# Performance work log

Measured on AMD Instinct MI355X. Metric: run time of the kernel, lower is better.

Reference implementation:

```python
import jax, jax.numpy as jnp
import numpy as np

NUM_LAYERS = 4
HID = 512
BATCH = 32
SEQ = 2048


def log_g(x):
    # log of the g() activation used by minGRU: g(x) = x+0.5 for x>=0, sigmoid(x) for x<0
    return jnp.where(x >= 0, jnp.log(jax.nn.relu(x) + 0.5), -jax.nn.softplus(-x))


def parallel_scan_log(log_coeffs, log_values):
    # log_coeffs: (B, T, H), log_values: (B, T+1, H); returns h: (B, T, H)
    a_star = jnp.cumsum(jnp.pad(log_coeffs, ((0, 0), (1, 0), (0, 0))), axis=1)  # (B, T+1, H)
    log_h = a_star + jax.lax.cumlogsumexp(log_values - a_star, axis=1)
    return jnp.exp(log_h)[:, 1:]


def setup_inputs() -> dict:
    key = jax.random.key(0)
    ks = jax.random.split(key, 4)
    x = jax.random.normal(ks[0], (BATCH, SEQ, HID), dtype=jnp.float32)
    h0 = jax.random.uniform(ks[1], (NUM_LAYERS, BATCH, HID), dtype=jnp.float32)
    scale = 0.02
    Wz = jax.random.normal(ks[2], (NUM_LAYERS, HID, HID), dtype=jnp.float32) * scale
    Wh = jax.random.normal(ks[3], (NUM_LAYERS, HID, HID), dtype=jnp.float32) * scale
    bz = jnp.zeros((NUM_LAYERS, HID), dtype=jnp.float32)
    bh = jnp.zeros((NUM_LAYERS, HID), dtype=jnp.float32)
    gamma = jnp.ones((NUM_LAYERS, HID), dtype=jnp.float32)
    beta = jnp.zeros((NUM_LAYERS, HID), dtype=jnp.float32)
    return {"x": x, "h0": h0, "Wz": Wz, "bz": bz, "Wh": Wh, "bh": bh, "gamma": gamma, "beta": beta}


def layernorm(x, g, b, eps=1e-5):
    mu = jnp.mean(x, axis=-1, keepdims=True)
    var = jnp.mean((x - mu) ** 2, axis=-1, keepdims=True)
    return (x - mu) * jax.lax.rsqrt(var + eps) * g + b


def reference(x, h0, Wz, bz, Wh, bh, gamma, beta):
    cur = x
    hiddens = []
    L = Wz.shape[0]
    for i in range(L):
        k = jnp.einsum('btd,dh->bth', cur, Wz[i]) + bz[i]
        log_z = -jax.nn.softplus(-k)          # log(sigmoid(k)) = log(z)
        log_coeffs = -jax.nn.softplus(k)      # log(1-z)
        log_tilde_h = log_g(jnp.einsum('btd,dh->bth', cur, Wh[i]) + bh[i])
        log_h0 = log_g(h0[i])[:, None, :]     # (B, 1, H)
        log_values = jnp.concatenate([log_h0, log_z + log_tilde_h], axis=1)
        h = parallel_scan_log(log_coeffs, log_values)  # (B, T, H)
        hiddens.append(h[:, -1])
        out = layernorm(h, gamma[i], beta[i])
        cur = out + cur  # res_proj is Identity since input_size == hidden_size
    return cur, jnp.stack(hiddens, axis=0)
```

## Files before the change

### kernel.cpp

```cpp
#include <hip/hip_runtime.h>
#include <stdint.h>

typedef unsigned short u16;
typedef __bf16 bf16x8 __attribute__((ext_vector_type(8)));
typedef float f32x4 __attribute__((ext_vector_type(4)));

#define HID 512
#define BATCH 32
#define SEQ 2048
#define NLAYERS 4
#define BT (BATCH*SEQ)
#define CHUNKS 64
#define TC (SEQ/CHUNKS)

__device__ __forceinline__ float bf2f(uint32_t lo) {
  union { uint32_t u; float f; } c; c.u = lo << 16; return c.f;
}
__device__ __forceinline__ uint32_t f2bf(float f) {
  union { float f; uint32_t u; } c; c.f = f;
  return (c.u + 0x7fffu + ((c.u >> 16) & 1u)) >> 16;
}
__device__ __forceinline__ float fast_rcp(float x) { return __builtin_amdgcn_rcpf(x); }

__device__ __forceinline__ void gload_lds16(const u16* g, u16* l) {
  __builtin_amdgcn_global_load_lds((__attribute__((address_space(1))) void*)g,
                                   (__attribute__((address_space(3))) void*)l, 16, 0, 0);
}

__global__ __launch_bounds__(256) void conv_weights(const float* __restrict__ Wz,
                                                    const float* __restrict__ Wh,
                                                    u16* __restrict__ Wt) {
  __shared__ float tile[64][65];
  const int l = blockIdx.z;
  const int k0 = blockIdx.x * 64;
  const int n0 = blockIdx.y * 64;
  const float* W = (n0 < 512 ? Wz : Wh) + (size_t)l * HID * HID;
  const int nc0 = (n0 < 512) ? n0 : n0 - 512;
  const int tx = threadIdx.x & 63, ty = threadIdx.x >> 6;
  for (int r = ty; r < 64; r += 4) tile[r][tx] = W[(size_t)(k0 + r) * HID + nc0 + tx];
  __syncthreads();
  for (int r = ty; r < 64; r += 4)
    Wt[((size_t)l * 1024 + n0 + r) * HID + k0 + tx] = (u16)f2bf(tile[tx][r]);
}

__global__ __launch_bounds__(256) void conv_x(const float* __restrict__ x, u16* __restrict__ xb) {
  size_t i = ((size_t)blockIdx.x * 256 + threadIdx.x) * 4;
  float4 f = *(const float4*)(x + i);
  uint2 o;
  o.x = f2bf(f.x) | (f2bf(f.y) << 16);
  o.y = f2bf(f.z) | (f2bf(f.w) << 16);
  *(uint2*)(xb + i) = o;
}

__global__ __launch_bounds__(256) void gemm_av(const u16* __restrict__ Ab,
                                               const u16* __restrict__ Btw,
                                               const float* __restrict__ bz,
                                               const float* __restrict__ bh,
                                               uint32_t* __restrict__ av,
                                               float* __restrict__ Ac,
                                               float* __restrict__ Bc) {
  __shared__ u16 As[128 * 32];
  __shared__ u16 Bs[128 * 32];
  const int blk = blockIdx.x;
  const int sub = blk & 63;
  const int hb = sub >> 3;
  const int mt = (blk >> 6) * 8 + (sub & 7);
  const int m0 = mt * 128;
  const int tid = threadIdx.x;
  const int lane = tid & 63;
  const int wv = tid >> 6;

  f32x4 acc[2][8];
#pragma unroll
  for (int i = 0; i < 2; ++i)
#pragma unroll
    for (int j = 0; j < 8; ++j) acc[i][j] = (f32x4){0.f, 0.f, 0.f, 0.f};

  const int srow = wv * 32 + (lane >> 2);
  const int swz_st = (((lane & 3) ^ ((lane >> 3) & 3))) * 8;
  const u16* gA = Ab + (size_t)(m0 + srow) * HID + swz_st;
  const int nn = srow;
  const int brow = (nn < 64) ? (hb * 64 + nn) : (448 + hb * 64 + nn);
  const u16* gB = Btw + (size_t)brow * HID + swz_st;

  const int rdoff = (((lane >> 4) ^ ((lane >> 1) & 3))) * 8;

  for (int kk = 0; kk < HID; kk += 32) {
#pragma unroll
    for (int j = 0; j < 2; ++j) {
      gload_lds16(gA + (size_t)(j * 16) * HID + kk, &As[(wv * 32 + j * 16) * 32]);
      gload_lds16(gB + (size_t)(j * 16) * HID + kk, &Bs[(wv * 32 + j * 16) * 32]);
    }
    __syncthreads();
    bf16x8 af[2], bfr[8];
#pragma unroll
    for (int i = 0; i < 2; ++i)
      af[i] = *(const bf16x8*)&As[(wv * 32 + i * 16 + (lane & 15)) * 32 + rdoff];
#pragma unroll
    for (int j = 0; j < 8; ++j)
      bfr[j] = *(const bf16x8*)&Bs[(j * 16 + (lane & 15)) * 32 + rdoff];
#pragma unroll
    for (int i = 0; i < 2; ++i)
#pragma unroll
      for (int j = 0; j < 8; ++j)
        acc[i][j] = __builtin_amdgcn_mfma_f32_16x16x32_bf16(af[i], bfr[j], acc[i][j], 0, 0, 0);
    __syncthreads();
  }

  const int col0 = hb * 64 + (lane & 15);
  const int quad = lane >> 4;
  float bzv[4], bhv[4];
#pragma unroll
  for (int jj = 0; jj < 4; ++jj) { bzv[jj] = bz[col0 + jj * 16]; bhv[jj] = bh[col0 + jj * 16]; }

  const int mrow = m0;
  const int wrow = mrow + wv * 32;
  const int bb = wrow >> 11;
  const int cc = (wrow & 2047) >> 5;
  const size_t abase = ((size_t)(bb * CHUNKS + cc)) * HID;

#pragma unroll
  for (int jj = 0; jj < 4; ++jj) {
    float Aseg[2], Bseg[2];
#pragma unroll
    for (int i = 0; i < 2; ++i) {
      const int rbase = wrow + i * 16 + quad * 4;
      float A = 1.f, Bv = 0.f;
#pragma unroll
      for (int r = 0; r < 4; ++r) {
        float kv = acc[i][jj][r] + bzv[jj];
        float hv = acc[i][jj + 4][r] + bhv[jj];
        float e = __expf(-kv);
        float inv = fast_rcp(1.f + e);
        float a = e * inv;
        float v = inv * ((hv >= 0.f) ? (hv + 0.5f) : fast_rcp(1.f + __expf(-hv)));
        av[(size_t)(rbase + r) * HID + col0 + jj * 16] = f2bf(a) | (f2bf(v) << 16);
        A *= a;
        Bv = a * Bv + v;
      }
      Aseg[i] = A; Bseg[i] = Bv;
    }
#pragma unroll
    for (int i = 0; i < 2; ++i) {
      float Ap = __shfl_xor(Aseg[i], 16), Bp = __shfl_xor(Bseg[i], 16);
      float Ae = (quad & 1) ? Ap : Aseg[i], Be = (quad & 1) ? Bp : Bseg[i];
      float Al = (quad & 1) ? Aseg[i] : Ap, Bl = (quad & 1) ? Bseg[i] : Bp;
      Aseg[i] = Al * Ae; Bseg[i] = Al * Be + Bl;
      Ap = __shfl_xor(Aseg[i], 32); Bp = __shfl_xor(Bseg[i], 32);
      Ae = (quad & 2) ? Ap : Aseg[i]; Be = (quad & 2) ? Bp : Bseg[i];
      Al = (quad & 2) ? Aseg[i] : Ap; Bl = (quad & 2) ? Bseg[i] : Bp;
      Aseg[i] = Al * Ae; Bseg[i] = Al * Be + Bl;
    }
    float CA = Aseg[1] * Aseg[0];
    float CB = Aseg[1] * Bseg[0] + Bseg[1];
    if (quad == 0) {
      Ac[abase + col0 + jj * 16] = CA;
      Bc[abase + col0 + jj * 16] = CB;
    }
  }
}

__global__ __launch_bounds__(256) void scan_boundary(const float* __restrict__ Ac,
                                                     const float* __restrict__ Bc,
                                                     const float* __restrict__ h0,
                                                     float* __restrict__ hinit,
                                                     float* __restrict__ hid_out) {
  const int idx = blockIdx.x * 256 + threadIdx.x;
  const int b = idx >> 9, h = idx & 511;
  float x0 = h0[idx];
  float hr = (x0 >= 0.f) ? (x0 + 0.5f) : fast_rcp(1.f + __expf(-x0));
  for (int c = 0; c < CHUNKS; ++c) {
    size_t o = ((size_t)(b * CHUNKS + c)) * HID + h;
    hinit[o] = hr;
    hr = Ac[o] * hr + Bc[o];
  }
  hid_out[idx] = hr;
}

__global__ __launch_bounds__(512) void scan_apply(const uint32_t* av,
                                                  const float* __restrict__ hinit,
                                                  const u16* __restrict__ resb,
                                                  const float* __restrict__ gamma,
                                                  const float* __restrict__ beta,
                                                  u16* outb, float* outf) {
  __shared__ float hbuf[TC][HID];
  const int b = blockIdx.y, c = blockIdx.x, h = threadIdx.x;
  const int lane = h & 63, wv = h >> 6;
  const size_t rowbase = (size_t)(b * SEQ + c * TC) * HID;

  float hr = hinit[((size_t)(b * CHUNKS + c)) * HID + h];
#pragma unroll 8
  for (int t = 0; t < TC; ++t) {
    uint32_t p = av[rowbase + (size_t)t * HID + h];
    hr = bf2f(p & 0xffffu) * hr + bf2f(p >> 16);
    hbuf[t][h] = hr;
  }
  __syncthreads();

  const int h0c = lane * 8;
  const f32x4 gm0 = *(const f32x4*)&gamma[h0c];
  const f32x4 gm1 = *(const f32x4*)&gamma[h0c + 4];
  const f32x4 be0 = *(const f32x4*)&beta[h0c];
  const f32x4 be1 = *(const f32x4*)&beta[h0c + 4];
#pragma unroll
  for (int i = 0; i < 4; ++i) {
    const int t = wv * 4 + i;
    f32x4 v0 = *(const f32x4*)&hbuf[t][h0c];
    f32x4 v1 = *(const f32x4*)&hbuf[t][h0c + 4];
    float s = v0[0] + v0[1] + v0[2] + v0[3] + v1[0] + v1[1] + v1[2] + v1[3];
    float q = v0[0]*v0[0] + v0[1]*v0[1] + v0[2]*v0[2] + v0[3]*v0[3]
            + v1[0]*v1[0] + v1[1]*v1[1] + v1[2]*v1[2] + v1[3]*v1[3];
#pragma unroll
    for (int d = 32; d; d >>= 1) { s += __shfl_xor(s, d); q += __shfl_xor(q, d); }
    const float mu = s * (1.f / HID);
    const float rs = rsqrtf(q * (1.f / HID) - mu * mu + 1e-5f);
    const size_t o = rowbase + (size_t)t * HID + h0c;
    uint4 rr = *(const uint4*)(resb + o);
    float y[8];
    const uint32_t rw[4] = {rr.x, rr.y, rr.z, rr.w};
#pragma unroll
    for (int j = 0; j < 8; ++j) {
      float hv = (j < 4) ? v0[j] : v1[j - 4];
      float gmv = (j < 4) ? gm0[j] : gm1[j - 4];
      float bev = (j < 4) ? be0[j] : be1[j - 4];
      float rv = bf2f((rw[j >> 1] >> ((j & 1) * 16)) & 0xffffu);
      y[j] = (hv - mu) * rs * gmv + bev + rv;
    }
    if (outb) {
      uint4 ob;
      ob.x = f2bf(y[0]) | (f2bf(y[1]) << 16);
      ob.y = f2bf(y[2]) | (f2bf(y[3]) << 16);
      ob.z = f2bf(y[4]) | (f2bf(y[5]) << 16);
      ob.w = f2bf(y[6]) | (f2bf(y[7]) << 16);
      *(uint4*)(outb + o) = ob;
    }
    if (outf) {
      f32x4 o0 = {y[0], y[1], y[2], y[3]}, o1 = {y[4], y[5], y[6], y[7]};
      *(f32x4*)(outf + o) = o0;
      *(f32x4*)(outf + o + 4) = o1;
    }
  }
}

extern "C" void kernel_launch(void* const* d_in, const int* in_sizes, int n_in,
                              void* d_out, int out_size, void* d_ws, size_t ws_size,
                              hipStream_t stream) {
  (void)in_sizes; (void)n_in; (void)out_size; (void)ws_size;
  const float* x     = (const float*)d_in[0];
  const float* h0    = (const float*)d_in[1];
  const float* Wz    = (const float*)d_in[2];
  const float* bz    = (const float*)d_in[3];
  const float* Wh    = (const float*)d_in[4];
  const float* bh    = (const float*)d_in[5];
  const float* gamma = (const float*)d_in[6];
  const float* beta  = (const float*)d_in[7];

  float* outf = (float*)d_out;
  uint32_t* av = (uint32_t*)d_out;

  char* ws = (char*)d_ws;
  u16* curb = (u16*)ws;                                   size_t off = (size_t)BT * HID * 2;
  u16* Wt = (u16*)(ws + off);                             off += (size_t)NLAYERS * 1024 * HID * 2;
  float* Ac = (float*)(ws + off);                         off += (size_t)BATCH * CHUNKS * HID * 4;
  float* Bc = (float*)(ws + off);                         off += (size_t)BATCH * CHUNKS * HID * 4;
  float* hinit = (float*)(ws + off);

  hipLaunchKernelGGL(conv_weights, dim3(8, 16, NLAYERS), dim3(256), 0, stream, Wz, Wh, Wt);
  hipLaunchKernelGGL(conv_x, dim3(BT * HID / 1024), dim3(256), 0, stream, x, curb);

  for (int l = 0; l < NLAYERS; ++l) {
    const bool last = (l == NLAYERS - 1);
    hipLaunchKernelGGL(gemm_av, dim3(4096), dim3(256), 0, stream,
                       curb, Wt + (size_t)l * 1024 * HID, bz + l * HID, bh + l * HID,
                       av, Ac, Bc);
    hipLaunchKernelGGL(scan_boundary, dim3(BATCH * HID / 256), dim3(256), 0, stream,
                       Ac, Bc, h0 + (size_t)l * BATCH * HID, hinit,
                       outf + (size_t)BT * HID + (size_t)l * BATCH * HID);
    hipLaunchKernelGGL(scan_apply, dim3(CHUNKS, BATCH), dim3(512), 0, stream,
                       av, hinit, curb, gamma + l * HID, beta + l * HID,
                       last ? nullptr : curb, last ? outf : nullptr);
  }
}
```

Baseline: 819.0 us.

## Rewrite gated GEMM with 256x256 tiles, double-buffered LDS and phased MFMA pipeline

Replaces the 128x128 tile, single-buffered GEMM with a 512-thread block computing a 256-row by 256-column (128 z + 128 h) tile. It uses double-buffered LDS with async global-to-LDS loads interleaved between MFMA phases, plus explicit barriers, waitcnt and setprio scheduling. The XCD-aware block mapping is revised. The aim is to hide global load latency, raise arithmetic intensity per LDS byte and cut redundant A/B fetches, at the cost of much larger LDS use (128KB) and register pressure, which lowers occupancy.

```diff
diff --git a/kernel.cpp b/kernel.cpp
--- a/kernel.cpp
+++ b/kernel.cpp
@@ -52,112 +52,174 @@
   *(uint2*)(xb + i) = o;
 }
 
-__global__ __launch_bounds__(256) void gemm_av(const u16* __restrict__ Ab,
+__global__ __launch_bounds__(512) void gemm_av(const u16* __restrict__ Ab,
                                                const u16* __restrict__ Btw,
                                                const float* __restrict__ bz,
-                                               const float* __restrict__ bh,
+                                               const float* __restrict__ bhp,
                                                uint32_t* __restrict__ av,
                                                float* __restrict__ Ac,
                                                float* __restrict__ Bc) {
-  __shared__ u16 As[128 * 32];
-  __shared__ u16 Bs[128 * 32];
-  const int blk = blockIdx.x;
-  const int sub = blk & 63;
-  const int hb = sub >> 3;
-  const int mt = (blk >> 6) * 8 + (sub & 7);
-  const int m0 = mt * 128;
+  __shared__ __align__(16) u16 As[2][2][8192];
+  __shared__ __align__(16) u16 Bs[2][2][8192];
+
+  const int bid = blockIdx.x;
+  const int xcd = bid & 7, rr_ = bid >> 3;
+  const int mt = (rr_ >> 2) * 8 + xcd;
+  const int nt = rr_ & 3;
+  const int m0 = mt * 256;
+
   const int tid = threadIdx.x;
-  const int lane = tid & 63;
-  const int wv = tid >> 6;
-
-  f32x4 acc[2][8];
-#pragma unroll
-  for (int i = 0; i < 2; ++i)
-#pragma unroll
-    for (int j = 0; j < 8; ++j) acc[i][j] = (f32x4){0.f, 0.f, 0.f, 0.f};
-
-  const int srow = wv * 32 + (lane >> 2);
-  const int swz_st = (((lane & 3) ^ ((lane >> 3) & 3))) * 8;
-  const u16* gA = Ab + (size_t)(m0 + srow) * HID + swz_st;
-  const int nn = srow;
-  const int brow = (nn < 64) ? (hb * 64 + nn) : (448 + hb * 64 + nn);
-  const u16* gB = Btw + (size_t)brow * HID + swz_st;
-
-  const int rdoff = (((lane >> 4) ^ ((lane >> 1) & 3))) * 8;
-
-  for (int kk = 0; kk < HID; kk += 32) {
-#pragma unroll
-    for (int j = 0; j < 2; ++j) {
-      gload_lds16(gA + (size_t)(j * 16) * HID + kk, &As[(wv * 32 + j * 16) * 32]);
-      gload_lds16(gB + (size_t)(j * 16) * HID + kk, &Bs[(wv * 32 + j * 16) * 32]);
+  const int lane = tid & 63, wv = tid >> 6;
+  const int wm = wv >> 2, wn = wv & 3;
+  const int l15 = lane & 15, quad = lane >> 4;
+  const int rx = l15 & 7;
+  const int bhalf = wn >> 1;
+
+  const int aro0 = l15 * 64 + ((quad ^ rx) * 8);
+  const int aro1 = l15 * 64 + (((4 + quad) ^ rx) * 8);
+  const int bro0 = ((wn & 1) * 64 + l15) * 64 + ((quad ^ rx) * 8);
+  const int bro1 = ((wn & 1) * 64 + l15) * 64 + (((4 + quad) ^ rx) * 8);
+
+  const int srow = tid >> 3;
+  const int kslot = (lane & 7) ^ (srow & 7);
+  const u16* aS = Ab + (size_t)(m0 + srow) * HID + kslot * 8;
+  const int qb = (srow >> 5) & 1, jb = srow & 31;
+  const u16* bS = Btw + (size_t)(qb * 512 + nt * 128 + jb) * HID + kslot * 8;
+
+  f32x4 acc[8][4];
+#pragma unroll
+  for (int i = 0; i < 8; ++i)
+#pragma unroll
+    for (int j = 0; j < 4; ++j) acc[i][j] = (f32x4){0.f, 0.f, 0.f, 0.f};
+  bf16x8 afr[4][2], bfr[4][2];
+
+#define STG_A(T, H, D) if ((T) < 8) { \
+    gload_lds16(aS + (size_t)((H)*65536 + (T)*64), &As[D][H][wv*512]); \
+    gload_lds16(aS + (size_t)((H)*65536 + 32768 + (T)*64), &As[D][H][4096 + wv*512]); }
+#define STG_B(T, H, D) if ((T) < 8) { \
+    gload_lds16(bS + (size_t)((H)*32768 + (T)*64), &Bs[D][H][wv*512]); \
+    gload_lds16(bS + (size_t)((H)*32768 + 16384 + (T)*64), &Bs[D][H][4096 + wv*512]); }
+#define LDA4(D, MB) { \
+    _Pragma("unroll") for (int m_ = 0; m_ < 4; ++m_) \
+    _Pragma("unroll") for (int k_ = 0; k_ < 2; ++k_) \
+      afr[m_][k_] = *(const bf16x8*)&As[D][wm][((MB)+m_)*1024 + (k_ ? aro1 : aro0)]; }
+#define LDB2(D, NB) { \
+    _Pragma("unroll") for (int n_ = 0; n_ < 2; ++n_) \
+    _Pragma("unroll") for (int k_ = 0; k_ < 2; ++k_) \
+      bfr[(NB)+n_][k_] = *(const bf16x8*)&Bs[D][bhalf][((NB)+n_)*1024 + (k_ ? bro1 : bro0)]; }
+#define QUAD(MB, NB) { \
+    _Pragma("unroll") for (int k_ = 0; k_ < 2; ++k_) \
+    _Pragma("unroll") for (int m_ = 0; m_ < 4; ++m_) \
+    _Pragma("unroll") for (int n_ = 0; n_ < 2; ++n_) \
+      acc[(MB)+m_][(NB)+n_] = __builtin_amdgcn_mfma_f32_16x16x32_bf16( \
+          afr[m_][k_], bfr[(NB)+n_][k_], acc[(MB)+m_][(NB)+n_], 0, 0, 0); }
+#define PH_MID \
+    __builtin_amdgcn_s_barrier(); \
+    asm volatile("s_waitcnt lgkmcnt(0)" ::: "memory"); \
+    __builtin_amdgcn_sched_barrier(0); \
+    __builtin_amdgcn_s_setprio(1);
+#define PH_END \
+    __builtin_amdgcn_s_setprio(0); \
+    __builtin_amdgcn_s_barrier(); \
+    __builtin_amdgcn_sched_barrier(0);
+#define PH_END_VM(N) \
+    __builtin_amdgcn_s_setprio(0); \
+    asm volatile("s_waitcnt vmcnt(" #N ")" ::: "memory"); \
+    __builtin_amdgcn_s_barrier(); \
+    __builtin_amdgcn_sched_barrier(0);
+
+  STG_A(0, 0, 0); STG_A(0, 1, 0);
+  STG_B(0, 0, 0); STG_B(0, 1, 0);
+  STG_B(1, 0, 1); STG_B(1, 1, 1);
+  asm volatile("s_waitcnt vmcnt(4)" ::: "memory");
+  __builtin_amdgcn_s_barrier();
+  __builtin_amdgcn_sched_barrier(0);
+
+#pragma unroll
+  for (int it = 0; it < 4; ++it) {
+    const int ta = 2 * it, tb = 2 * it + 1;
+    LDA4(0, 0); LDB2(0, 0); STG_A(tb, 0, 1);
+    PH_MID; QUAD(0, 0); PH_END;
+    LDB2(0, 2); STG_A(tb, 1, 1);
+    PH_MID; QUAD(0, 2); PH_END;
+    LDA4(0, 4); STG_B(ta + 2, 0, 0);
+    PH_MID; QUAD(4, 0); PH_END;
+    STG_B(ta + 2, 1, 0);
+    PH_MID; QUAD(4, 2);
+    if (it == 3) { PH_END_VM(0); } else { PH_END_VM(4); }
+    LDA4(1, 0); LDB2(1, 0); STG_A(ta + 2, 0, 0);
+    PH_MID; QUAD(0, 0); PH_END;
+    LDB2(1, 2); STG_A(ta + 2, 1, 0);
+    PH_MID; QUAD(0, 2); PH_END;
+    LDA4(1, 4); STG_B(tb + 2, 0, 1);
+    PH_MID; QUAD(4, 0); PH_END;
+    STG_B(tb + 2, 1, 1);
+    PH_MID; QUAD(4, 2); PH_END_VM(4);
+  }
+
+  const int colbase = nt * 128 + wn * 32;
+  float bzv[2], bhv[2];
+#pragma unroll
+  for (int nf = 0; nf < 2; ++nf) {
+    bzv[nf] = bz[colbase + nf * 16 + l15];
+    bhv[nf] = bhp[colbase + nf * 16 + l15];
+  }
+  const int wrow0 = m0 + wm * 128;
+  const int bb = wrow0 >> 11;
+#pragma unroll
+  for (int c = 0; c < 4; ++c) {
+    const int cc = ((wrow0 + c * 32) & 2047) >> 5;
+    const size_t abase = (size_t)(bb * CHUNKS + cc) * HID;
+#pragma unroll
+    for (int nf = 0; nf < 2; ++nf) {
+      const int col = colbase + nf * 16 + l15;
+      float Aseg[2], Bseg[2];
+#pragma unroll
+      for (int hseg = 0; hseg < 2; ++hseg) {
+        const int mf = 2 * c + hseg;
+        const int rbase = wrow0 + mf * 16 + quad * 4;
+        float A = 1.f, Bv = 0.f;
+#pragma unroll
+        for (int r = 0; r < 4; ++r) {
+          float kv = acc[mf][nf][r] + bzv[nf];
+          float hv = acc[mf][nf + 2][r] + bhv[nf];
+          float e = __expf(-kv);
+          float inv = fast_rcp(1.f + e);
+          float a = e * inv;
+          float v = inv * ((hv >= 0.f) ? (hv + 0.5f) : fast_rcp(1.f + __expf(-hv)));
+          av[(size_t)(rbase + r) * HID + col] = f2bf(a) | (f2bf(v) << 16);
+          A *= a;
+          Bv = a * Bv + v;
+        }
+        Aseg[hseg] = A; Bseg[hseg] = Bv;
+      }
+#pragma unroll
+      for (int hseg = 0; hseg < 2; ++hseg) {
+        float Ap = __shfl_xor(Aseg[hseg], 16), Bp = __shfl_xor(Bseg[hseg], 16);
+        float Ae = (quad & 1) ? Ap : Aseg[hseg], Be = (quad & 1) ? Bp : Bseg[hseg];
+        float Al = (quad & 1) ? Aseg[hseg] : Ap, Bl = (quad & 1) ? Bseg[hseg] : Bp;
+        Aseg[hseg] = Al * Ae; Bseg[hseg] = Al * Be + Bl;
+        Ap = __shfl_xor(Aseg[hseg], 32); Bp = __shfl_xor(Bseg[hseg], 32);
+        Ae = (quad & 2) ? Ap : Aseg[hseg]; Be = (quad & 2) ? Bp : Bseg[hseg];
+        Al = (quad & 2) ? Aseg[hseg] : Ap; Bl = (quad & 2) ? Bseg[hseg] : Bp;
+        Aseg[hseg] = Al * Ae; Bseg[hseg] = Al * Be + Bl;
+      }
+      float CA = Aseg[1] * Aseg[0];
+      float CB = Aseg[1] * Bseg[0] + Bseg[1];
+      if (quad == 0) {
+        Ac[abase + col] = CA;
+        Bc[abase + col] = CB;
+      }
     }
-    __syncthreads();
-    bf16x8 af[2], bfr[8];
-#pragma unroll
-    for (int i = 0; i < 2; ++i)
-      af[i] = *(const bf16x8*)&As[(wv * 32 + i * 16 + (lane & 15)) * 32 + rdoff];
-#pragma unroll
-    for (int j = 0; j < 8; ++j)
-      bfr[j] = *(const bf16x8*)&Bs[(j * 16 + (lane & 15)) * 32 + rdoff];
-#pragma unroll
-    for (int i = 0; i < 2; ++i)
-#pragma unroll
-      for (int j = 0; j < 8; ++j)
-        acc[i][j] = __builtin_amdgcn_mfma_f32_16x16x32_bf16(af[i], bfr[j], acc[i][j], 0, 0, 0);
-    __syncthreads();
-  }
-
-  const int col0 = hb * 64 + (lane & 15);
-  const int quad = lane >> 4;
-  float bzv[4], bhv[4];
-#pragma unroll
-  for (int jj = 0; jj < 4; ++jj) { bzv[jj] = bz[col0 + jj * 16]; bhv[jj] = bh[col0 + jj * 16]; }
-
-  const int mrow = m0;
-  const int wrow = mrow + wv * 32;
-  const int bb = wrow >> 11;
-  const int cc = (wrow & 2047) >> 5;
-  const size_t abase = ((size_t)(bb * CHUNKS + cc)) * HID;
-
-#pragma unroll
-  for (int jj = 0; jj < 4; ++jj) {
-    float Aseg[2], Bseg[2];
-#pragma unroll
-    for (int i = 0; i < 2; ++i) {
-      const int rbase = wrow + i * 16 + quad * 4;
-      float A = 1.f, Bv = 0.f;
-#pragma unroll
-      for (int r = 0; r < 4; ++r) {
-        float kv = acc[i][jj][r] + bzv[jj];
-        float hv = acc[i][jj + 4][r] + bhv[jj];
-        float e = __expf(-kv);
-        float inv = fast_rcp(1.f + e);
-        float a = e * inv;
-        float v = inv * ((hv >= 0.f) ? (hv + 0.5f) : fast_rcp(1.f + __expf(-hv)));
-        av[(size_t)(rbase + r) * HID + col0 + jj * 16] = f2bf(a) | (f2bf(v) << 16);
-        A *= a;
-        Bv = a * Bv + v;
-      }
-      Aseg[i] = A; Bseg[i] = Bv;
-    }
-#pragma unroll
-    for (int i = 0; i < 2; ++i) {
-      float Ap = __shfl_xor(Aseg[i], 16), Bp = __shfl_xor(Bseg[i], 16);
-      float Ae = (quad & 1) ? Ap : Aseg[i], Be = (quad & 1) ? Bp : Bseg[i];
-      float Al = (quad & 1) ? Aseg[i] : Ap, Bl = (quad & 1) ? Bseg[i] : Bp;
-      Aseg[i] = Al * Ae; Bseg[i] = Al * Be + Bl;
-      Ap = __shfl_xor(Aseg[i], 32); Bp = __shfl_xor(Bseg[i], 32);
-      Ae = (quad & 2) ? Ap : Aseg[i]; Be = (quad & 2) ? Bp : Bseg[i];
-      Al = (quad & 2) ? Aseg[i] : Ap; Bl = (quad & 2) ? Bseg[i] : Bp;
-      Aseg[i] = Al * Ae; Bseg[i] = Al * Be + Bl;
-    }
-    float CA = Aseg[1] * Aseg[0];
-    float CB = Aseg[1] * Bseg[0] + Bseg[1];
-    if (quad == 0) {
-      Ac[abase + col0 + jj * 16] = CA;
-      Bc[abase + col0 + jj * 16] = CB;
-    }
-  }
+  }
+#undef STG_A
+#undef STG_B
+#undef LDA4
+#undef LDB2
+#undef QUAD
+#undef PH_MID
+#undef PH_END
+#undef PH_END_VM
 }
 
 __global__ __launch_bounds__(256) void scan_boundary(const float* __restrict__ Ac,
@@ -270,7 +332,7 @@
 
   for (int l = 0; l < NLAYERS; ++l) {
     const bool last = (l == NLAYERS - 1);
-    hipLaunchKernelGGL(gemm_av, dim3(4096), dim3(256), 0, stream,
+    hipLaunchKernelGGL(gemm_av, dim3(1024), dim3(512), 0, stream,
                        curb, Wt + (size_t)l * 1024 * HID, bz + l * HID, bh + l * HID,
                        av, Ac, Bc);
     hipLaunchKernelGGL(scan_boundary, dim3(BATCH * HID / 256), dim3(256), 0, stream,
```

Measured after the change: 825.4 us. No clear change (+0.8%).

## Restructure gemm_av to stage full-K A tile in LDS and stream B from global

Applied to the files above, without the earlier changes.

The GEMM now has each 512-thread block own 64 rows and all 1024 output columns. The full 64x512 A tile is loaded into swizzled LDS once, while B fragments are read straight from global memory with register double-buffering, which removes the per-K-step barriers. This targets the synchronisation overhead and the repeated A reloads of the old 128x128 tiling. In exchange it uses more registers (acc 4x8 plus double-buffered fragments) and relies on cache hits for B. Separately, the bf16 packing switches to the hardware v_cvt_pk_bf16_f32 instruction in place of manual rounding.

```diff
diff --git a/kernel.cpp b/kernel.cpp
--- a/kernel.cpp
+++ b/kernel.cpp
@@ -19,6 +19,11 @@
 __device__ __forceinline__ uint32_t f2bf(float f) {
   union { float f; uint32_t u; } c; c.f = f;
   return (c.u + 0x7fffu + ((c.u >> 16) & 1u)) >> 16;
+}
+__device__ __forceinline__ uint32_t pk_bf16(float lo, float hi) {
+  uint32_t r;
+  asm("v_cvt_pk_bf16_f32 %0, %1, %2" : "=v"(r) : "v"(lo), "v"(hi));
+  return r;
 }
 __device__ __forceinline__ float fast_rcp(float x) { return __builtin_amdgcn_rcpf(x); }
 
@@ -47,115 +52,124 @@
   size_t i = ((size_t)blockIdx.x * 256 + threadIdx.x) * 4;
   float4 f = *(const float4*)(x + i);
   uint2 o;
-  o.x = f2bf(f.x) | (f2bf(f.y) << 16);
-  o.y = f2bf(f.z) | (f2bf(f.w) << 16);
+  o.x = pk_bf16(f.x, f.y);
+  o.y = pk_bf16(f.z, f.w);
   *(uint2*)(xb + i) = o;
 }
 
-__global__ __launch_bounds__(256) void gemm_av(const u16* __restrict__ Ab,
+__global__ __launch_bounds__(512) void gemm_av(const u16* __restrict__ Ab,
                                                const u16* __restrict__ Btw,
                                                const float* __restrict__ bz,
-                                               const float* __restrict__ bh,
+                                               const float* __restrict__ bhp,
                                                uint32_t* __restrict__ av,
                                                float* __restrict__ Ac,
                                                float* __restrict__ Bc) {
-  __shared__ u16 As[128 * 32];
-  __shared__ u16 Bs[128 * 32];
-  const int blk = blockIdx.x;
-  const int sub = blk & 63;
-  const int hb = sub >> 3;
-  const int mt = (blk >> 6) * 8 + (sub & 7);
-  const int m0 = mt * 128;
+  __shared__ __align__(16) u16 As[64 * 512];
+
+  const int bid = blockIdx.x;
+  const int m0 = bid * 64;
   const int tid = threadIdx.x;
-  const int lane = tid & 63;
-  const int wv = tid >> 6;
-
-  f32x4 acc[2][8];
-#pragma unroll
-  for (int i = 0; i < 2; ++i)
+  const int lane = tid & 63, wv = tid >> 6;
+  const int l15 = lane & 15, quad = lane >> 4;
+  const int r7 = l15 & 7;
+
+#pragma unroll
+  for (int r = 0; r < 8; ++r) {
+    const int row = r * 8 + wv;
+    gload_lds16(Ab + (size_t)(m0 + row) * HID + (size_t)((lane ^ (row & 7)) * 8),
+                &As[row * 512]);
+  }
+
+  const u16* bp[8];
+#pragma unroll
+  for (int j = 0; j < 8; ++j) {
+    const int brow = (j < 4) ? (wv * 64 + j * 16 + l15)
+                             : (512 + wv * 64 + (j - 4) * 16 + l15);
+    bp[j] = Btw + (size_t)brow * HID + quad * 8;
+  }
+
+  f32x4 acc[4][8];
+#pragma unroll
+  for (int i = 0; i < 4; ++i)
 #pragma unroll
     for (int j = 0; j < 8; ++j) acc[i][j] = (f32x4){0.f, 0.f, 0.f, 0.f};
-
-  const int srow = wv * 32 + (lane >> 2);
-  const int swz_st = (((lane & 3) ^ ((lane >> 3) & 3))) * 8;
-  const u16* gA = Ab + (size_t)(m0 + srow) * HID + swz_st;
-  const int nn = srow;
-  const int brow = (nn < 64) ? (hb * 64 + nn) : (448 + hb * 64 + nn);
-  const u16* gB = Btw + (size_t)brow * HID + swz_st;
-
-  const int rdoff = (((lane >> 4) ^ ((lane >> 1) & 3))) * 8;
-
-  for (int kk = 0; kk < HID; kk += 32) {
-#pragma unroll
-    for (int j = 0; j < 2; ++j) {
-      gload_lds16(gA + (size_t)(j * 16) * HID + kk, &As[(wv * 32 + j * 16) * 32]);
-      gload_lds16(gB + (size_t)(j * 16) * HID + kk, &Bs[(wv * 32 + j * 16) * 32]);
-    }
-    __syncthreads();
-    bf16x8 af[2], bfr[8];
-#pragma unroll
-    for (int i = 0; i < 2; ++i)
-      af[i] = *(const bf16x8*)&As[(wv * 32 + i * 16 + (lane & 15)) * 32 + rdoff];
-#pragma unroll
-    for (int j = 0; j < 8; ++j)
-      bfr[j] = *(const bf16x8*)&Bs[(j * 16 + (lane & 15)) * 32 + rdoff];
-#pragma unroll
-    for (int i = 0; i < 2; ++i)
+  bf16x8 af[2][4], bfr[2][8];
+
+#define PFA(P, KS) { _Pragma("unroll") for (int i_ = 0; i_ < 4; ++i_) \
+    af[P][i_] = *(const bf16x8*)&As[(i_ * 16 + l15) * 512 + ((((KS) * 4 + quad) ^ r7) * 8)]; }
+#define PFB(P, KS) { _Pragma("unroll") for (int j_ = 0; j_ < 8; ++j_) \
+    bfr[P][j_] = *(const bf16x8*)(bp[j_] + (KS) * 32); }
+
+  PFB(0, 0);
+  __syncthreads();
+  PFA(0, 0);
+
+#pragma unroll
+  for (int ks = 0; ks < 16; ++ks) {
+    const int cur = ks & 1, nxt = cur ^ 1;
+    if (ks < 15) { PFB(nxt, ks + 1); PFA(nxt, ks + 1); }
+#pragma unroll
+    for (int i = 0; i < 4; ++i)
 #pragma unroll
       for (int j = 0; j < 8; ++j)
-        acc[i][j] = __builtin_amdgcn_mfma_f32_16x16x32_bf16(af[i], bfr[j], acc[i][j], 0, 0, 0);
-    __syncthreads();
-  }
-
-  const int col0 = hb * 64 + (lane & 15);
-  const int quad = lane >> 4;
+        acc[i][j] = __builtin_amdgcn_mfma_f32_16x16x32_bf16(af[cur][i], bfr[cur][j],
+                                                            acc[i][j], 0, 0, 0);
+  }
+#undef PFA
+#undef PFB
+
+  const int colbase = wv * 64;
   float bzv[4], bhv[4];
 #pragma unroll
-  for (int jj = 0; jj < 4; ++jj) { bzv[jj] = bz[col0 + jj * 16]; bhv[jj] = bh[col0 + jj * 16]; }
-
-  const int mrow = m0;
-  const int wrow = mrow + wv * 32;
-  const int bb = wrow >> 11;
-  const int cc = (wrow & 2047) >> 5;
-  const size_t abase = ((size_t)(bb * CHUNKS + cc)) * HID;
-
-#pragma unroll
   for (int jj = 0; jj < 4; ++jj) {
-    float Aseg[2], Bseg[2];
-#pragma unroll
-    for (int i = 0; i < 2; ++i) {
-      const int rbase = wrow + i * 16 + quad * 4;
-      float A = 1.f, Bv = 0.f;
-#pragma unroll
-      for (int r = 0; r < 4; ++r) {
-        float kv = acc[i][jj][r] + bzv[jj];
-        float hv = acc[i][jj + 4][r] + bhv[jj];
-        float e = __expf(-kv);
-        float inv = fast_rcp(1.f + e);
-        float a = e * inv;
-        float v = inv * ((hv >= 0.f) ? (hv + 0.5f) : fast_rcp(1.f + __expf(-hv)));
-        av[(size_t)(rbase + r) * HID + col0 + jj * 16] = f2bf(a) | (f2bf(v) << 16);
-        A *= a;
-        Bv = a * Bv + v;
+    bzv[jj] = bz[colbase + jj * 16 + l15];
+    bhv[jj] = bhp[colbase + jj * 16 + l15];
+  }
+  const int bb = m0 >> 11;
+#pragma unroll
+  for (int c = 0; c < 2; ++c) {
+    const int cc = ((m0 & 2047) >> 5) + c;
+    const size_t abase = (size_t)(bb * CHUNKS + cc) * HID;
+#pragma unroll
+    for (int jj = 0; jj < 4; ++jj) {
+      const int col = colbase + jj * 16 + l15;
+      float Aseg[2], Bseg[2];
+#pragma unroll
+      for (int hseg = 0; hseg < 2; ++hseg) {
+        const int mf = 2 * c + hseg;
+        const int rbase = m0 + mf * 16 + quad * 4;
+        float A = 1.f, Bv = 0.f;
+#pragma unroll
+        for (int r = 0; r < 4; ++r) {
+          float kv = acc[mf][jj][r] + bzv[jj];
+          float hv = acc[mf][jj + 4][r] + bhv[jj];
+          float e = __expf(-kv);
+          float inv = fast_rcp(1.f + e);
+          float a = e * inv;
+          float v = inv * ((hv >= 0.f) ? (hv + 0.5f) : fast_rcp(1.f + __expf(-hv)));
+          av[(size_t)(rbase + r) * HID + col] = pk_bf16(a, v);
+          A *= a;
+          Bv = a * Bv + v;
+        }
+        Aseg[hseg] = A; Bseg[hseg] = Bv;
       }
-      Aseg[i] = A; Bseg[i] = Bv;
-    }
-#pragma unroll
-    for (int i = 0; i < 2; ++i) {
-      float Ap = __shfl_xor(Aseg[i], 16), Bp = __shfl_xor(Bseg[i], 16);
-      float Ae = (quad & 1) ? Ap : Aseg[i], Be = (quad & 1) ? Bp : Bseg[i];
-      float Al = (quad & 1) ? Aseg[i] : Ap, Bl = (quad & 1) ? Bseg[i] : Bp;
-      Aseg[i] = Al * Ae; Bseg[i] = Al * Be + Bl;
-      Ap = __shfl_xor(Aseg[i], 32); Bp = __shfl_xor(Bseg[i], 32);
-      Ae = (quad & 2) ? Ap : Aseg[i]; Be = (quad & 2) ? Bp : Bseg[i];
-      Al = (quad & 2) ? Aseg[i] : Ap; Bl = (quad & 2) ? Bseg[i] : Bp;
-      Aseg[i] = Al * Ae; Bseg[i] = Al * Be + Bl;
-    }
-    float CA = Aseg[1] * Aseg[0];
-    float CB = Aseg[1] * Bseg[0] + Bseg[1];
-    if (quad == 0) {
-      Ac[abase + col0 + jj * 16] = CA;
-      Bc[abase + col0 + jj * 16] = CB;
+#pragma unroll
+      for (int hseg = 0; hseg < 2; ++hseg) {
+        float Ap = __shfl_xor(Aseg[hseg], 16), Bp = __shfl_xor(Bseg[hseg], 16);
+        float Ae = (quad & 1) ? Ap : Aseg[hseg], Be = (quad & 1) ? Bp : Bseg[hseg];
+        float Al = (quad & 1) ? Aseg[hseg] : Ap, Bl = (quad & 1) ? Bseg[hseg] : Bp;
+        Aseg[hseg] = Al * Ae; Bseg[hseg] = Al * Be + Bl;
+        Ap = __shfl_xor(Aseg[hseg], 32); Bp = __shfl_xor(Bseg[hseg], 32);
+        Ae = (quad & 2) ? Ap : Aseg[hseg]; Be = (quad & 2) ? Bp : Bseg[hseg];
+        Al = (quad & 2) ? Aseg[hseg] : Ap; Bl = (quad & 2) ? Bseg[hseg] : Bp;
+        Aseg[hseg] = Al * Ae; Bseg[hseg] = Al * Be + Bl;
+      }
+      float CA = Aseg[1] * Aseg[0];
+      float CB = Aseg[1] * Bseg[0] + Bseg[1];
+      if (quad == 0) {
+        Ac[abase + col] = CA;
+        Bc[abase + col] = CB;
+      }
     }
   }
 }
@@ -228,10 +242,10 @@
     }
     if (outb) {
       uint4 ob;
-      ob.x = f2bf(y[0]) | (f2bf(y[1]) << 16);
-      ob.y = f2bf(y[2]) | (f2bf(y[3]) << 16);
-      ob.z = f2bf(y[4]) | (f2bf(y[5]) << 16);
-      ob.w = f2bf(y[6]) | (f2bf(y[7]) << 16);
+      ob.x = pk_bf16(y[0], y[1]);
+      ob.y = pk_bf16(y[2], y[3]);
+      ob.z = pk_bf16(y[4], y[5]);
+      ob.w = pk_bf16(y[6], y[7]);
       *(uint4*)(outb + o) = ob;
     }
     if (outf) {
@@ -270,7 +284,7 @@
 
   for (int l = 0; l < NLAYERS; ++l) {
     const bool last = (l == NLAYERS - 1);
-    hipLaunchKernelGGL(gemm_av, dim3(4096), dim3(256), 0, stream,
+    hipLaunchKernelGGL(gemm_av, dim3(BT / 64), dim3(512), 0, stream,
                        curb, Wt + (size_t)l * 1024 * HID, bz + l * HID, bh + l * HID,
                        av, Ac, Bc);
     hipLaunchKernelGGL(scan_boundary, dim3(BATCH * HID / 256), dim3(256), 0, stream,
```

New measurement: 1.041 ms. +27.1%, slower.
